# Performance work log

Measured on AMD Instinct MI355X. Metric: run time of the kernel, lower is better.

Reference implementation:

```python
import jax, jax.numpy as jnp
import numpy as np

N_NODES = 10000
N_EDGES = 320000
N_TYPES = 64
EDGE_INV = 8
MULT = 32          # env_embed_multiplicity
LAT = 256          # latent MLP width
SH_DIM = 9         # l = 0,1,2 -> 1+3+5
L_OFF = (0, 1, 4)
L_DIM = (1, 3, 5)
R_MAX = 6.0
POLY_P = 6.0
AVG_NEIGH = 32.0


def _w(key, fan_in, fan_out):
    return jax.random.normal(key, (fan_in, fan_out), jnp.float32) / np.sqrt(fan_in)


def setup_inputs() -> dict:
    key = jax.random.key(0)
    ks = jax.random.split(key, 20)
    return {
        "edge_attr": jax.random.normal(ks[0], (N_EDGES, SH_DIM), jnp.float32),
        "edge_length": jax.random.uniform(ks[1], (N_EDGES,), jnp.float32),
        "edge_invariants": jax.random.normal(ks[2], (N_EDGES, EDGE_INV), jnp.float32),
        "node_invariants": jax.random.uniform(ks[3], (N_NODES, N_TYPES), jnp.float32),
        "W2a": _w(ks[4], 2 * N_TYPES + EDGE_INV, LAT),
        "W2b": _w(ks[5], LAT, LAT),
        "Wl1a": _w(ks[6], LAT + MULT * 3, LAT),
        "Wl1b": _w(ks[7], LAT, LAT),
        "Wenv0": _w(ks[8], LAT, 2 * MULT * 3),
        "Wenv1": _w(ks[9], LAT, MULT * 3),
        "Wenvlin": jax.random.normal(ks[10], (2, 3, MULT, MULT), jnp.float32) / np.sqrt(MULT),
        "Wprod": jax.random.normal(ks[11], (2, 3, N_TYPES, MULT), jnp.float32) / np.sqrt(N_TYPES),
        "Wfeat": jax.random.normal(ks[12], (2, 3, MULT, MULT), jnp.float32) / np.sqrt(MULT),
        "Wfinlat": _w(ks[13], LAT, 3 * MULT * MULT),
        "Wro1": _w(ks[14], LAT + MULT * 3, LAT),
        "Wro2": _w(ks[15], LAT, 1),
        "edge_index": jax.random.randint(ks[16], (2, N_EDGES), 0, N_NODES),
    }


def poly_cutoff(x, p=POLY_P):
    # nequip polynomial cutoff, f(0)=1, f(1)=0 with p continuous derivatives
    f = (1.0 - (p + 1.0) * (p + 2.0) / 2.0 * x ** p
         + p * (p + 2.0) * x ** (p + 1.0)
         - p * (p + 1.0) / 2.0 * x ** (p + 2.0))
    return jnp.where(x < 1.0, f, 0.0)


def weight_channels(sh, w):
    # MakeWeightedChannels: sh [E,9], w [E,K,3 irreps] -> [E,K,9]
    return jnp.concatenate(
        [sh[:, None, o:o + d] * w[:, :, l:l + 1]
         for l, (o, d) in enumerate(zip(L_OFF, L_DIM))], axis=-1)


def mix_channels(x, W):
    # equivariant Linear: per-l channel mixing. x [N,K,9], W [3,K,K]
    return jnp.concatenate(
        [jnp.einsum('nkm,kj->njm', x[:, :, o:o + d], W[l])
         for l, (o, d) in enumerate(zip(L_OFF, L_DIM))], axis=-1)


def l_norms(x):
    # rotation-invariant per-(channel,l) norms: x [E,K,9] -> [E, K*3]
    return jnp.concatenate(
        [jnp.sqrt(jnp.sum(x[:, :, o:o + d] ** 2, axis=-1) + 1e-8)
         for (o, d) in zip(L_OFF, L_DIM)], axis=-1)


def _forward(edge_index, edge_attr, edge_length, edge_invariants, node_invariants,
             W2a, W2b, Wl1a, Wl1b, Wenv0, Wenv1, Wenvlin, Wprod, Wfeat,
             Wfinlat, Wro1, Wro2):
    center, neigh = edge_index[0], edge_index[1]
    n_nodes = node_invariants.shape[0]
    silu = jax.nn.silu
    cutoff = poly_cutoff(edge_length / R_MAX)                  # [E]
    alpha = jax.nn.sigmoid(0.0)                                # resnet update param init 0
    c_old = 1.0 / jnp.sqrt(alpha * alpha + 1.0)
    c_new = alpha * c_old
    norm = 1.0 / AVG_NEIGH                                     # env_sum_normalizations

    def env_and_product(env_w, lidx):
        # weighted SH channels -> scatter-sum env -> env linear -> product basis
        env_e = weight_channels(edge_attr, env_w) * cutoff[:, None, None]   # [E,K,9]
        env = jax.ops.segment_sum(env_e, center, num_segments=n_nodes) * norm
        env = mix_channels(env, Wenvlin[lidx])                  # [N,K,9]
        s = env[:, :, 0:1]                                      # scalar (l=0) channel
        ew = jnp.einsum('nt,ctk->nck', node_invariants, Wprod[lidx])  # element weights [N,3,K]
        prod = env * (ew[:, 0, :, None] + ew[:, 1, :, None] * s + ew[:, 2, :, None] * s * s)
        return mix_channels(prod, Wfeat[lidx])[center]          # gather back to edges [E,K,9]

    # ---- layer 0: two-body latent ----
    lat_in = jnp.concatenate(
        [node_invariants[center], node_invariants[neigh], edge_invariants], axis=-1)
    latents = cutoff[:, None] * silu(silu(lat_in @ W2a) @ W2b)  # [E,LAT]
    w_all = (latents @ Wenv0).reshape(-1, 2, MULT, 3)           # initial + env weights
    features0 = weight_channels(edge_attr, w_all[:, 0])         # initial weighted channels
    features = env_and_product(w_all[:, 1], 0)

    # ---- layer 1: latent resnet update ----
    lat_in = jnp.concatenate([latents, l_norms(features)], axis=-1)
    new_lat = silu(silu(lat_in @ Wl1a) @ Wl1b)
    latents = c_old * latents + c_new * cutoff[:, None] * new_lat
    features = env_and_product((latents @ Wenv1).reshape(-1, MULT, 3), 1)

    # ---- final per-edge linear (weights from latents) + diagonal 'uuu' TP -> invariants ----
    wfin = (latents @ Wfinlat).reshape(-1, 3, MULT, MULT)
    feat_fin = jnp.concatenate(
        [jnp.einsum('ekm,ekj->ejm', features[:, :, o:o + d], wfin[:, l])
         for l, (o, d) in enumerate(zip(L_OFF, L_DIM))], axis=-1)
    scal = jnp.concatenate(
        [jnp.sum(feat_fin[:, :, o:o + d] * features0[:, :, o:o + d], axis=-1)
         for (o, d) in zip(L_OFF, L_DIM)], axis=-1)              # [E, K*3]
    ro_in = jnp.concatenate([latents, scal], axis=-1)
    return silu(ro_in @ Wro1) @ Wro2                             # [E,1] edge energies


def reference(edge_attr, edge_length, edge_invariants, node_invariants,
              W2a, W2b, Wl1a, Wl1b, Wenv0, Wenv1, Wenvlin, Wprod, Wfeat,
              Wfinlat, Wro1, Wro2, edge_index):
    return _forward(edge_index, edge_attr, edge_length, edge_invariants, node_invariants,
                    W2a, W2b, Wl1a, Wl1b, Wenv0, Wenv1, Wenvlin, Wprod, Wfeat,
                    Wfinlat, Wro1, Wro2)
```

## Files before the change

### kernel.cpp

```cpp
#include <hip/hip_runtime.h>
#include <math.h>

#define NE 320000
#define NNODES 10000
#define EB 32
#define NBLK (NE / EB)
#define AST 360
#define BST 264
#define SST 98

typedef _Float16 f16x8 __attribute__((ext_vector_type(8)));
typedef float f32x4 __attribute__((ext_vector_type(4)));
typedef float f32x16 __attribute__((ext_vector_type(16)));

__device__ __forceinline__ float silu(float x) { return x / (1.0f + __expf(-x)); }
__device__ __forceinline__ float cutf(float len) {
    float x = len * (1.0f / 6.0f);
    float x2 = x * x, x6 = x2 * x2 * x2;
    float f = 1.0f - 28.0f * x6 + 48.0f * x6 * x - 21.0f * x6 * x2;
    return (x < 1.0f) ? f : 0.0f;
}

__global__ __launch_bounds__(256) void k_zero(float* __restrict__ p, int n) {
    int i = blockIdx.x * 256 + threadIdx.x;
    if (i < n) p[i] = 0.f;
}

__global__ __launch_bounds__(256) void k_packf(const float* __restrict__ src,
                                               _Float16* __restrict__ dst,
                                               int K, int KS, int NT, int stride,
                                               int colOff) {
    int i = blockIdx.x * 256 + threadIdx.x;
    if (i >= NT * KS * 512) return;
    int j = i & 7, lane = (i >> 3) & 63;
    int blk = i >> 9;
    int ks = blk % KS, nt = blk / KS;
    int k = ks * 32 + (lane >> 4) * 8 + j;
    int n = colOff + nt * 16 + (lane & 15);
    dst[i] = (k < K) ? (_Float16)src[(size_t)k * stride + n] : (_Float16)0.f;
}

__global__ __launch_bounds__(256) void k_packfin3(const float* __restrict__ W,
                                                  _Float16* __restrict__ dst) {
    int i = blockIdx.x * 256 + threadIdx.x;
    int j = i & 7, lane = (i >> 3) & 63, q = (i >> 9) & 15, s = i >> 13;
    int l = s >> 5, ke = s & 31;
    int c = q * 16 + (lane >> 5) * 8 + j;
    int n = l * 1024 + ke * 32 + (lane & 31);
    dst[i] = (_Float16)W[(size_t)c * 3072 + n];
}

__global__ __launch_bounds__(256) void k_packro5(const float* __restrict__ W,
                                                 _Float16* __restrict__ dst) {
    int i = blockIdx.x * 256 + threadIdx.x;
    if (i >= 90112) return;
    int j = i & 7, lane = (i >> 3) & 63, u = i >> 9;
    int cb = u / 22, ks2 = u - cb * 22;
    int k = ks2 * 16 + (lane >> 5) * 8 + j;
    int n = cb * 32 + (lane & 31);
    dst[i] = (_Float16)W[(size_t)k * 256 + n];
}

template <int NT>
__device__ __forceinline__ void mfma_gemm2(int ksteps, const _Float16* Ah, int astride,
                                           const _Float16* __restrict__ Wt, int t,
                                           f32x4* acc0, f32x4* acc1) {
    int wave = t >> 6, lane = t & 63, r = lane & 15, g = lane >> 4;
    const int TPW = (NT + 3) / 4;
#pragma unroll
    for (int i = 0; i < TPW; ++i) {
        acc0[i] = (f32x4){0.f, 0.f, 0.f, 0.f};
        acc1[i] = (f32x4){0.f, 0.f, 0.f, 0.f};
    }
    for (int ks = 0; ks < ksteps; ++ks) {
        f16x8 a0 = *(const f16x8*)(Ah + r * astride + ks * 32 + g * 8);
        f16x8 a1 = *(const f16x8*)(Ah + (16 + r) * astride + ks * 32 + g * 8);
#pragma unroll
        for (int i = 0; i < TPW; ++i) {
            int nt = wave + 4 * i;
            if (nt < NT) {
                f16x8 b = *(const f16x8*)(Wt + ((size_t)(nt * ksteps + ks) * 64 + lane) * 8);
                acc0[i] = __builtin_amdgcn_mfma_f32_16x16x32_f16(a0, b, acc0[i], 0, 0, 0);
                acc1[i] = __builtin_amdgcn_mfma_f32_16x16x32_f16(a1, b, acc1[i], 0, 0, 0);
            }
        }
    }
}

__device__ __forceinline__ void gather_latin(
    const float* __restrict__ nodeinv, const float* __restrict__ edgeinv,
    const float* __restrict__ elen, const int* __restrict__ eidx,
    int e0, int t, _Float16* Ah, float* s_cut) {
    if (t < EB) s_cut[t] = cutf(elen[e0 + t]);
    for (int i = t; i < EB * 160; i += 256) {
        int ee = i / 160, k = i - ee * 160;
        int e = e0 + ee;
        float v;
        if (k < 64)       v = nodeinv[eidx[e] * 64 + k];
        else if (k < 128) v = nodeinv[eidx[NE + e] * 64 + (k - 64)];
        else if (k < 136) v = edgeinv[(size_t)e * 8 + (k - 128)];
        else              v = 0.f;
        Ah[ee * AST + k] = (_Float16)v;
    }
}

__device__ __forceinline__ void lat0_mfma2(const _Float16* __restrict__ W2aT,
                                           const _Float16* __restrict__ W2bT,
                                           int t, _Float16* Ah, _Float16* AhB,
                                           const float* s_cut) {
    int wave = t >> 6, lane = t & 63, r = lane & 15, g = lane >> 4;
    f32x4 acc0[4], acc1[4];
    mfma_gemm2<16>(5, Ah, AST, W2aT, t, acc0, acc1);
#pragma unroll
    for (int i = 0; i < 4; ++i) {
        int nt = wave + 4 * i;
#pragma unroll
        for (int i2 = 0; i2 < 4; ++i2) {
            AhB[(g * 4 + i2) * BST + nt * 16 + r] = (_Float16)silu(acc0[i][i2]);
            AhB[(16 + g * 4 + i2) * BST + nt * 16 + r] = (_Float16)silu(acc1[i][i2]);
        }
    }
    __syncthreads();
    mfma_gemm2<16>(8, AhB, BST, W2bT, t, acc0, acc1);
#pragma unroll
    for (int i = 0; i < 4; ++i) {
        int nt = wave + 4 * i;
#pragma unroll
        for (int i2 = 0; i2 < 4; ++i2) {
            int ro = g * 4 + i2, col = nt * 16 + r;
            Ah[ro * AST + col] = (_Float16)(s_cut[ro] * silu(acc0[i][i2]));
            Ah[(16 + ro) * AST + col] = (_Float16)(s_cut[16 + ro] * silu(acc1[i][i2]));
        }
    }
    __syncthreads();
}

__device__ __forceinline__ void gather_lnorm(const float* __restrict__ featN,
                                             const int* __restrict__ eidx,
                                             int e0, int t, _Float16* Ah) {
    for (int i = t; i < EB * 96; i += 256) {
        int ee = i / 96, rem = i - ee * 96;
        int l = rem >> 5, kk = rem & 31;
        int off = (l == 0) ? 0 : ((l == 1) ? 1 : 4);
        int d = (l == 0) ? 1 : ((l == 1) ? 3 : 5);
        const float* f = featN + (size_t)eidx[e0 + ee] * 288 + kk;
        float s = 1e-8f;
        for (int mm = off; mm < off + d; ++mm) { float x = f[mm * 32]; s = fmaf(x, x, s); }
        Ah[ee * AST + 256 + rem] = (_Float16)sqrtf(s);
    }
}

__device__ __forceinline__ void scatter_env(const float* __restrict__ edge_attr,
                                            const int* __restrict__ eidx,
                                            const float* s_w, const float* s_cut,
                                            int e0, int t, float* __restrict__ env) {
    for (int i = t; i < EB * 32; i += 256) {
        int el = i >> 5, k = i & 31;
        int e = e0 + el;
        float cw = s_cut[el];
        int n = eidx[e];
        float w0 = s_w[el * 96 + k * 3 + 0] * cw;
        float w1 = s_w[el * 96 + k * 3 + 1] * cw;
        float w2 = s_w[el * 96 + k * 3 + 2] * cw;
        float* dst = env + (size_t)n * 288 + k;
#pragma unroll
        for (int m = 0; m < 9; ++m) {
            float w = (m == 0) ? w0 : ((m < 4) ? w1 : w2);
            atomicAdd(dst + m * 32, edge_attr[(size_t)e * 9 + m] * w);
        }
    }
}

__device__ __forceinline__ void epi6_f32(const f32x4* acc0, const f32x4* acc1, int t,
                                         float* s_w) {
    int wave = t >> 6, lane = t & 63, r = lane & 15, g = lane >> 4;
#pragma unroll
    for (int i = 0; i < 2; ++i) {
        int nt = wave + 4 * i;
        if (nt < 6) {
#pragma unroll
            for (int i2 = 0; i2 < 4; ++i2) {
                s_w[(g * 4 + i2) * 96 + nt * 16 + r] = acc0[i][i2];
                s_w[(16 + g * 4 + i2) * 96 + nt * 16 + r] = acc1[i][i2];
            }
        }
    }
}

__global__ __launch_bounds__(256) void k1_lat_scatter0(
    const float* __restrict__ nodeinv, const float* __restrict__ edgeinv,
    const float* __restrict__ elen, const float* __restrict__ edge_attr,
    const int* __restrict__ eidx, const _Float16* __restrict__ W2aT,
    const _Float16* __restrict__ W2bT, const _Float16* __restrict__ Wenv0T,
    float* __restrict__ env, _Float16* __restrict__ lat0h,
    _Float16* __restrict__ w0h) {
    __shared__ alignas(16) _Float16 Ah[EB * AST];
    __shared__ alignas(16) _Float16 AhB[EB * BST];
    __shared__ float s_cut[EB];
    float* s_w = (float*)AhB;
    int t = threadIdx.x;
    int e0 = blockIdx.x * EB;
    int wave = t >> 6, lane = t & 63, r = lane & 15, g = lane >> 4;
    gather_latin(nodeinv, edgeinv, elen, eidx, e0, t, Ah, s_cut);
    __syncthreads();
    lat0_mfma2(W2aT, W2bT, t, Ah, AhB, s_cut);
    for (int i = t; i < EB * 32; i += 256) {
        int ee = i >> 5, c8 = (i & 31) * 8;
        *(f16x8*)(lat0h + (size_t)(e0 + ee) * 256 + c8) =
            *(const f16x8*)(Ah + ee * AST + c8);
    }
    f32x4 acc0[3], acc1[3];
    mfma_gemm2<12>(8, Ah, AST, Wenv0T, t, acc0, acc1);
#pragma unroll
    for (int i = 0; i < 3; ++i) {
        int nt = wave + 4 * i;
        if (nt < 6) {
#pragma unroll
            for (int i2 = 0; i2 < 4; ++i2) {
                w0h[(size_t)(e0 + g * 4 + i2) * 96 + nt * 16 + r] = (_Float16)acc0[i][i2];
                w0h[(size_t)(e0 + 16 + g * 4 + i2) * 96 + nt * 16 + r] = (_Float16)acc1[i][i2];
            }
        } else {
#pragma unroll
            for (int i2 = 0; i2 < 4; ++i2) {
                s_w[(g * 4 + i2) * 96 + (nt - 6) * 16 + r] = acc0[i][i2];
                s_w[(16 + g * 4 + i2) * 96 + (nt - 6) * 16 + r] = acc1[i][i2];
            }
        }
    }
    __syncthreads();
    scatter_env(edge_attr, eidx, s_w, s_cut, e0, t, env);
}

__global__ __launch_bounds__(288) void k_node(
    const float* envin, const float* __restrict__ nodeinv,
    const float* __restrict__ Wenvlin, const float* __restrict__ Wprod,
    const float* __restrict__ Wfeat, float* featOut) {
    __shared__ float s_env[288];
    __shared__ float s_inv[64];
    __shared__ float s_mix[288];
    __shared__ float s_ew[96];
    int n = blockIdx.x;
    int t = threadIdx.x;
    s_env[t] = envin[(size_t)n * 288 + t] * (1.0f / 32.0f);
    if (t < 64) s_inv[t] = nodeinv[n * 64 + t];
    __syncthreads();
    int m = t >> 5, j = t & 31;
    int l = (m == 0) ? 0 : ((m < 4) ? 1 : 2);
    float a = 0.f;
    for (int k = 0; k < 32; ++k) a = fmaf(s_env[m * 32 + k], Wenvlin[l * 1024 + k * 32 + j], a);
    if (t < 96) {
        int c = t >> 5, jj = t & 31;
        float b = 0.f;
        for (int tt = 0; tt < 64; ++tt) b = fmaf(s_inv[tt], Wprod[c * 2048 + tt * 32 + jj], b);
        s_ew[t] = b;
    }
    s_mix[t] = a;
    __syncthreads();
    float s = s_mix[j];
    float p = s_mix[t] * (s_ew[j] + s_ew[32 + j] * s + s_ew[64 + j] * s * s);
    __syncthreads();
    s_env[t] = p;
    __syncthreads();
    float o = 0.f;
    for (int jl = 0; jl < 32; ++jl) o = fmaf(s_env[m * 32 + jl], Wfeat[l * 1024 + jl * 32 + j], o);
    featOut[(size_t)n * 288 + t] = o;
}

__global__ __launch_bounds__(256) void k3_update_scatter1(
    const float* __restrict__ elen, const float* __restrict__ edge_attr,
    const int* __restrict__ eidx, const _Float16* __restrict__ Wl1aT,
    const _Float16* __restrict__ Wl1bT, const _Float16* __restrict__ Wenv1T,
    const float* __restrict__ featN0, float* __restrict__ env,
    _Float16* __restrict__ lat01h) {
    __shared__ alignas(16) _Float16 Ah[EB * AST];
    __shared__ alignas(16) _Float16 AhB[EB * BST];
    __shared__ float s_cut[EB];
    float* s_w = (float*)AhB;
    int t = threadIdx.x;
    int e0 = blockIdx.x * EB;
    int wave = t >> 6, lane = t & 63, r = lane & 15, g = lane >> 4;
    if (t < EB) s_cut[t] = cutf(elen[e0 + t]);
    for (int i = t; i < EB * 32; i += 256) {
        int ee = i >> 5, c8 = (i & 31) * 8;
        *(f16x8*)(Ah + ee * AST + c8) =
            *(const f16x8*)(lat01h + (size_t)(e0 + ee) * 256 + c8);
    }
    gather_lnorm(featN0, eidx, e0, t, Ah);
    __syncthreads();
    f32x4 acc0[4], acc1[4];
    mfma_gemm2<16>(11, Ah, AST, Wl1aT, t, acc0, acc1);
#pragma unroll
    for (int i = 0; i < 4; ++i) {
        int nt = wave + 4 * i;
#pragma unroll
        for (int i2 = 0; i2 < 4; ++i2) {
            AhB[(g * 4 + i2) * BST + nt * 16 + r] = (_Float16)silu(acc0[i][i2]);
            AhB[(16 + g * 4 + i2) * BST + nt * 16 + r] = (_Float16)silu(acc1[i][i2]);
        }
    }
    __syncthreads();
    mfma_gemm2<16>(8, AhB, BST, Wl1bT, t, acc0, acc1);
#pragma unroll
    for (int i = 0; i < 4; ++i) {
        int nt = wave + 4 * i;
#pragma unroll
        for (int i2 = 0; i2 < 4; ++i2) {
            int ro = g * 4 + i2, col = nt * 16 + r;
            float v0 = 0.8944271909999159f * (float)Ah[ro * AST + col] +
                       0.4472135954999579f * s_cut[ro] * silu(acc0[i][i2]);
            _Float16 h0 = (_Float16)v0;
            Ah[ro * AST + col] = h0;
            lat01h[(size_t)(e0 + ro) * 256 + col] = h0;
            float v1 = 0.8944271909999159f * (float)Ah[(16 + ro) * AST + col] +
                       0.4472135954999579f * s_cut[16 + ro] * silu(acc1[i][i2]);
            _Float16 h1 = (_Float16)v1;
            Ah[(16 + ro) * AST + col] = h1;
            lat01h[(size_t)(e0 + 16 + ro) * 256 + col] = h1;
        }
    }
    __syncthreads();
    mfma_gemm2<6>(8, Ah, AST, Wenv1T, t, acc0, acc1);
    epi6_f32(acc0, acc1, t, s_w);
    __syncthreads();
    scatter_env(edge_attr, eidx, s_w, s_cut, e0, t, env);
}

#define FEB 128
__global__ __launch_bounds__(256) void k5_fast(
    const float* __restrict__ edge_attr, const int* __restrict__ eidx,
    const _Float16* __restrict__ lat1h, const _Float16* __restrict__ w0h,
    const _Float16* __restrict__ Bfin3, const _Float16* __restrict__ Wro1T32,
    const float* __restrict__ Wro2, const float* __restrict__ featN1,
    float* __restrict__ out) {
    __shared__ alignas(16) _Float16 Bst[2][8192];
    __shared__ alignas(16) _Float16 s_S[FEB * SST];
    int t = threadIdx.x;
    int e0 = blockIdx.x * FEB;
    int wave = t >> 6, lane = t & 63;
    int r31 = lane & 31, kh5 = lane >> 5;
    for (int i = t; i < FEB * 96; i += 256) {
        int ee = i / 96, rem = i - ee * 96;
        int l = rem >> 5, kk = rem & 31;
        int off = (l == 0) ? 0 : ((l == 1) ? 1 : 4);
        int d = (l == 0) ? 1 : ((l == 1) ? 3 : 5);
        int e = e0 + ee;
        const float* f = featN1 + (size_t)eidx[e] * 288 + kk;
        float s = 0.f;
        for (int mm = off; mm < off + d; ++mm)
            s = fmaf(f[mm * 32], edge_attr[(size_t)e * 9 + mm], s);
        s_S[ee * SST + rem] = (_Float16)s;
    }
    f16x8 a2[16];
#pragma unroll
    for (int q = 0; q < 16; ++q)
        a2[q] = *(const f16x8*)(lat1h + (size_t)(e0 + wave * 32 + r31) * 256 +
                                q * 16 + kh5 * 8);
#pragma unroll
    for (int c = 0; c < 4; ++c) {
        f16x8 gc = *(const f16x8*)(Bfin3 + (size_t)(c * 256 + t) * 8);
        *(f16x8*)&Bst[0][(c * 256 + t) * 8] = gc;
    }
    __syncthreads();
    const f32x16 z16 = {0.f, 0.f, 0.f, 0.f, 0.f, 0.f, 0.f, 0.f,
                        0.f, 0.f, 0.f, 0.f, 0.f, 0.f, 0.f, 0.f};
    f32x16 acc[3];
#pragma unroll
    for (int l = 0; l < 3; ++l) acc[l] = z16;
    int cur = 0;
#pragma unroll
    for (int l = 0; l < 3; ++l) {
#pragma unroll 1
        for (int ke = 0; ke < 32; ++ke) {
            int s = l * 32 + ke;
            f16x8 g0, g1, g2, g3;
            if (s < 95) {
                const _Float16* g = Bfin3 + (size_t)(s + 1) * 8192;
                g0 = *(const f16x8*)(g + (size_t)(0 * 256 + t) * 8);
                g1 = *(const f16x8*)(g + (size_t)(1 * 256 + t) * 8);
                g2 = *(const f16x8*)(g + (size_t)(2 * 256 + t) * 8);
                g3 = *(const f16x8*)(g + (size_t)(3 * 256 + t) * 8);
            }
            _Float16 sh = s_S[(wave * 32 + r31) * SST + l * 32 + ke];
            f16x8 sb = {sh, sh, sh, sh, sh, sh, sh, sh};
#pragma unroll
            for (int q = 0; q < 16; ++q) {
                f16x8 b = *(const f16x8*)&Bst[cur][q * 512 + lane * 8];
                f16x8 ap = a2[q] * sb;
                acc[l] = __builtin_amdgcn_mfma_f32_32x32x16_f16(ap, b, acc[l], 0, 0, 0);
            }
            if (s < 95) {
                *(f16x8*)&Bst[cur ^ 1][(0 * 256 + t) * 8] = g0;
                *(f16x8*)&Bst[cur ^ 1][(1 * 256 + t) * 8] = g1;
                *(f16x8*)&Bst[cur ^ 1][(2 * 256 + t) * 8] = g2;
                *(f16x8*)&Bst[cur ^ 1][(3 * 256 + t) * 8] = g3;
            }
            __syncthreads();
            cur ^= 1;
        }
    }
#pragma unroll
    for (int l = 0; l < 3; ++l) {
#pragma unroll
        for (int reg = 0; reg < 16; ++reg) {
            int row = (reg & 3) + 8 * (reg >> 2) + 4 * kh5;
            int jo = r31;
            float w0 = (float)w0h[(size_t)(e0 + wave * 32 + row) * 96 + jo * 3 + l];
            s_S[(wave * 32 + row) * SST + l * 32 + jo] = (_Float16)(acc[l][reg] * w0);
        }
    }
    __syncthreads();
    float v16[16];
#pragma unroll
    for (int reg = 0; reg < 16; ++reg) v16[reg] = 0.f;
#pragma unroll 1
    for (int cb = 0; cb < 8; ++cb) {
        f32x16 racc = z16;
#pragma unroll
        for (int ks2 = 0; ks2 < 22; ++ks2) {
            f16x8 af = (ks2 < 16)
                ? a2[ks2]
                : *(const f16x8*)&s_S[(wave * 32 + r31) * SST + (ks2 - 16) * 16 + kh5 * 8];
            f16x8 b = *(const f16x8*)(Wro1T32 + ((size_t)(cb * 22 + ks2) * 512 + lane * 8));
            racc = __builtin_amdgcn_mfma_f32_32x32x16_f16(af, b, racc, 0, 0, 0);
        }
        float w2 = Wro2[cb * 32 + r31];
#pragma unroll
        for (int reg = 0; reg < 16; ++reg) v16[reg] += silu(racc[reg]) * w2;
    }
#pragma unroll
    for (int off = 1; off < 32; off <<= 1)
#pragma unroll
        for (int reg = 0; reg < 16; ++reg) v16[reg] += __shfl_xor(v16[reg], off);
    if (r31 == 0) {
#pragma unroll
        for (int reg = 0; reg < 16; ++reg) {
            int row = (reg & 3) + 8 * (reg >> 2) + 4 * kh5;
            out[e0 + wave * 32 + row] = v16[reg];
        }
    }
}

extern "C" void kernel_launch(void* const* d_in, const int* in_sizes, int n_in,
                              void* d_out, int out_size, void* d_ws, size_t ws_size,
                              hipStream_t stream) {
    (void)in_sizes; (void)n_in; (void)out_size;
    const float* edge_attr = (const float*)d_in[0];
    const float* edge_len  = (const float*)d_in[1];
    const float* edge_inv  = (const float*)d_in[2];
    const float* node_inv  = (const float*)d_in[3];
    const float* W2a     = (const float*)d_in[4];
    const float* W2b     = (const float*)d_in[5];
    const float* Wl1a    = (const float*)d_in[6];
    const float* Wl1b    = (const float*)d_in[7];
    const float* Wenv0   = (const float*)d_in[8];
    const float* Wenv1   = (const float*)d_in[9];
    const float* Wenvlin = (const float*)d_in[10];
    const float* Wprod   = (const float*)d_in[11];
    const float* Wfeat   = (const float*)d_in[12];
    const float* Wfinlat = (const float*)d_in[13];
    const float* Wro1    = (const float*)d_in[14];
    const float* Wro2    = (const float*)d_in[15];
    const int* eidx      = (const int*)d_in[16];
    float* out = (float*)d_out;

    _Float16* p = (_Float16*)d_ws;
    _Float16* Bfin3   = p; p += 786432;
    _Float16* W2aT    = p; p += 40960;
    _Float16* W2bT    = p; p += 65536;
    _Float16* Wenv0T  = p; p += 49152;
    _Float16* Wenv1T  = p; p += 24576;
    _Float16* Wl1aT   = p; p += 90112;
    _Float16* Wl1bT   = p; p += 65536;
    _Float16* Wro1T32 = p; p += 90112;
    float* env    = (float*)p;
    float* featN0 = env + (size_t)NNODES * 288;
    char* after = (char*)(featN0 + (size_t)NNODES * 288);
    size_t need_base = (size_t)(after - (char*)d_ws);
    if (ws_size < need_base) return;
    _Float16* lat01h = (_Float16*)after;
    _Float16* w0h    = lat01h + (size_t)NE * 256;
    size_t need = need_base + (size_t)NE * (256 + 96) * sizeof(_Float16);
    if (ws_size < need) return;

    const int ENV_N = NNODES * 288;
    k_packfin3<<<3072, 256, 0, stream>>>(Wfinlat, Bfin3);
    k_packf<<<160, 256, 0, stream>>>(W2a, W2aT, 136, 5, 16, 256, 0);
    k_packf<<<256, 256, 0, stream>>>(W2b, W2bT, 256, 8, 16, 256, 0);
    k_packf<<<192, 256, 0, stream>>>(Wenv0, Wenv0T, 256, 8, 12, 192, 0);
    k_packf<<<96, 256, 0, stream>>>(Wenv1, Wenv1T, 256, 8, 6, 96, 0);
    k_packf<<<352, 256, 0, stream>>>(Wl1a, Wl1aT, 352, 11, 16, 256, 0);
    k_packf<<<256, 256, 0, stream>>>(Wl1b, Wl1bT, 256, 8, 16, 256, 0);
    k_packro5<<<352, 256, 0, stream>>>(Wro1, Wro1T32);

    k_zero<<<(ENV_N + 255) / 256, 256, 0, stream>>>(env, ENV_N);
    k1_lat_scatter0<<<NBLK, 256, 0, stream>>>(node_inv, edge_inv, edge_len, edge_attr,
                                              eidx, W2aT, W2bT, Wenv0T, env, lat01h, w0h);
    k_node<<<NNODES, 288, 0, stream>>>(env, node_inv, Wenvlin, Wprod, Wfeat, featN0);
    k_zero<<<(ENV_N + 255) / 256, 256, 0, stream>>>(env, ENV_N);
    k3_update_scatter1<<<NBLK, 256, 0, stream>>>(edge_len, edge_attr, eidx,
                                                 Wl1aT, Wl1bT, Wenv1T, featN0, env, lat01h);
    k_node<<<NNODES, 288, 0, stream>>>(env, node_inv, Wenvlin + 3072, Wprod + 6144,
                                       Wfeat + 3072, env);
    k5_fast<<<NE / FEB, 256, 0, stream>>>(edge_attr, eidx, lat01h, w0h, Bfin3, Wro1T32,
                                          Wro2, env, out);
}
```

Measured before the change: 2.684 ms.

## Sort edges by source node to cut scatter atomics via segmented reduction

Adds a counting sort of edges by source node (histogram, scan, place), so every edge kernel works in sorted order. The env scatter in k1 and k3 then does a run-length segmented reduction in shared memory and issues one atomic per node run instead of one per edge. The goal is fewer global atomics and more locality in the gathers. The k5 inner loop is also changed to apply the per-channel scalar in fp32 after the MFMA, not by scaling the fp16 operand. The cost is extra sort kernels, indirect index loads, and a serial single-block scan.

New measurement: 2.685 ms, median of 2. About the same (+0.0%).

```diff
diff --git a/kernel.cpp b/kernel.cpp
--- a/kernel.cpp
+++ b/kernel.cpp
@@ -24,6 +24,54 @@
 __global__ __launch_bounds__(256) void k_zero(float* __restrict__ p, int n) {
     int i = blockIdx.x * 256 + threadIdx.x;
     if (i < n) p[i] = 0.f;
+}
+
+__global__ __launch_bounds__(256) void k_hist(const int* __restrict__ eidx,
+                                              int* __restrict__ cnt) {
+    int e = blockIdx.x * 256 + threadIdx.x;
+    if (e < NE) atomicAdd(&cnt[eidx[e]], 1);
+}
+
+__global__ __launch_bounds__(256) void k_scan(const int* __restrict__ cnt,
+                                              int* __restrict__ seg,
+                                              int* __restrict__ cursor) {
+    __shared__ int part[256];
+    __shared__ int base[256];
+    int t = threadIdx.x;
+    int start = t * 40;
+    int s = 0;
+    for (int i = 0; i < 40; ++i) {
+        int idx = start + i;
+        if (idx < NNODES) s += cnt[idx];
+    }
+    part[t] = s;
+    __syncthreads();
+    if (t == 0) {
+        int run = 0;
+        for (int i = 0; i < 256; ++i) { base[i] = run; run += part[i]; }
+    }
+    __syncthreads();
+    int run = base[t];
+    for (int i = 0; i < 40; ++i) {
+        int idx = start + i;
+        if (idx < NNODES) {
+            int c = cnt[idx];
+            seg[idx] = run;
+            cursor[idx] = run;
+            run += c;
+        }
+    }
+    if (t == 0) seg[NNODES] = NE;
+}
+
+__global__ __launch_bounds__(256) void k_place(const int* __restrict__ eidx,
+                                               int* __restrict__ cursor,
+                                               int* __restrict__ eord) {
+    int e = blockIdx.x * 256 + threadIdx.x;
+    if (e < NE) {
+        int p = atomicAdd(&cursor[eidx[e]], 1);
+        eord[p] = e;
+    }
 }
 
 __global__ __launch_bounds__(256) void k_packf(const float* __restrict__ src,
@@ -90,11 +138,14 @@
 __device__ __forceinline__ void gather_latin(
     const float* __restrict__ nodeinv, const float* __restrict__ edgeinv,
     const float* __restrict__ elen, const int* __restrict__ eidx,
-    int e0, int t, _Float16* Ah, float* s_cut) {
-    if (t < EB) s_cut[t] = cutf(elen[e0 + t]);
+    const int* __restrict__ eord, int e0, int t, _Float16* Ah, float* s_cut) {
+    if (t < EB) {
+        int e = eord ? eord[e0 + t] : (e0 + t);
+        s_cut[t] = cutf(elen[e]);
+    }
     for (int i = t; i < EB * 160; i += 256) {
         int ee = i / 160, k = i - ee * 160;
-        int e = e0 + ee;
+        int e = eord ? eord[e0 + ee] : (e0 + ee);
         float v;
         if (k < 64)       v = nodeinv[eidx[e] * 64 + k];
         else if (k < 128) v = nodeinv[eidx[NE + e] * 64 + (k - 64)];
@@ -137,13 +188,15 @@
 
 __device__ __forceinline__ void gather_lnorm(const float* __restrict__ featN,
                                              const int* __restrict__ eidx,
+                                             const int* __restrict__ eord,
                                              int e0, int t, _Float16* Ah) {
     for (int i = t; i < EB * 96; i += 256) {
         int ee = i / 96, rem = i - ee * 96;
         int l = rem >> 5, kk = rem & 31;
         int off = (l == 0) ? 0 : ((l == 1) ? 1 : 4);
         int d = (l == 0) ? 1 : ((l == 1) ? 3 : 5);
-        const float* f = featN + (size_t)eidx[e0 + ee] * 288 + kk;
+        int e = eord ? eord[e0 + ee] : (e0 + ee);
+        const float* f = featN + (size_t)eidx[e] * 288 + kk;
         float s = 1e-8f;
         for (int mm = off; mm < off + d; ++mm) { float x = f[mm * 32]; s = fmaf(x, x, s); }
         Ah[ee * AST + 256 + rem] = (_Float16)sqrtf(s);
@@ -171,6 +224,27 @@
     }
 }
 
+__device__ __forceinline__ void scatter_sorted(const float* s_sh, const int* s_nid,
+                                               const float* s_w, int t,
+                                               float* __restrict__ env) {
+    for (int pp = t; pp < 288; pp += 256) {
+        int m = pp >> 5, k = pp & 31;
+        int l = (m == 0) ? 0 : ((m < 4) ? 1 : 2);
+        float run = 0.f;
+        int nprev = s_nid[0];
+        for (int el = 0; el < EB; ++el) {
+            int nid = s_nid[el];
+            if (nid != nprev) {
+                atomicAdd(&env[(size_t)nprev * 288 + m * 32 + k], run);
+                run = 0.f;
+                nprev = nid;
+            }
+            run = fmaf(s_sh[el * 9 + m], s_w[el * 96 + k * 3 + l], run);
+        }
+        atomicAdd(&env[(size_t)nprev * 288 + m * 32 + k], run);
+    }
+}
+
 __device__ __forceinline__ void epi6_f32(const f32x4* acc0, const f32x4* acc1, int t,
                                          float* s_w) {
     int wave = t >> 6, lane = t & 63, r = lane & 15, g = lane >> 4;
@@ -193,15 +267,17 @@
     const int* __restrict__ eidx, const _Float16* __restrict__ W2aT,
     const _Float16* __restrict__ W2bT, const _Float16* __restrict__ Wenv0T,
     float* __restrict__ env, _Float16* __restrict__ lat0h,
-    _Float16* __restrict__ w0h) {
+    _Float16* __restrict__ w0h, const int* __restrict__ eord) {
     __shared__ alignas(16) _Float16 Ah[EB * AST];
     __shared__ alignas(16) _Float16 AhB[EB * BST];
     __shared__ float s_cut[EB];
+    __shared__ float s_sh[EB * 9];
+    __shared__ int s_nid[EB];
     float* s_w = (float*)AhB;
     int t = threadIdx.x;
     int e0 = blockIdx.x * EB;
     int wave = t >> 6, lane = t & 63, r = lane & 15, g = lane >> 4;
-    gather_latin(nodeinv, edgeinv, elen, eidx, e0, t, Ah, s_cut);
+    gather_latin(nodeinv, edgeinv, elen, eidx, eord, e0, t, Ah, s_cut);
     __syncthreads();
     lat0_mfma2(W2aT, W2bT, t, Ah, AhB, s_cut);
     for (int i = t; i < EB * 32; i += 256) {
@@ -228,8 +304,16 @@
             }
         }
     }
-    __syncthreads();
-    scatter_env(edge_attr, eidx, s_w, s_cut, e0, t, env);
+    if (eord) {
+        if (t < EB) s_nid[t] = eidx[eord[e0 + t]];
+        for (int i = t; i < EB * 9; i += 256) {
+            int el = i / 9, m = i - el * 9;
+            s_sh[i] = edge_attr[(size_t)eord[e0 + el] * 9 + m] * s_cut[el];
+        }
+    }
+    __syncthreads();
+    if (eord) scatter_sorted(s_sh, s_nid, s_w, t, env);
+    else      scatter_env(edge_attr, eidx, s_w, s_cut, e0, t, env);
 }
 
 __global__ __launch_bounds__(288) void k_node(
@@ -272,21 +356,26 @@
     const int* __restrict__ eidx, const _Float16* __restrict__ Wl1aT,
     const _Float16* __restrict__ Wl1bT, const _Float16* __restrict__ Wenv1T,
     const float* __restrict__ featN0, float* __restrict__ env,
-    _Float16* __restrict__ lat01h) {
+    _Float16* __restrict__ lat01h, const int* __restrict__ eord) {
     __shared__ alignas(16) _Float16 Ah[EB * AST];
     __shared__ alignas(16) _Float16 AhB[EB * BST];
     __shared__ float s_cut[EB];
+    __shared__ float s_sh[EB * 9];
+    __shared__ int s_nid[EB];
     float* s_w = (float*)AhB;
     int t = threadIdx.x;
     int e0 = blockIdx.x * EB;
     int wave = t >> 6, lane = t & 63, r = lane & 15, g = lane >> 4;
-    if (t < EB) s_cut[t] = cutf(elen[e0 + t]);
+    if (t < EB) {
+        int e = eord ? eord[e0 + t] : (e0 + t);
+        s_cut[t] = cutf(elen[e]);
+    }
     for (int i = t; i < EB * 32; i += 256) {
         int ee = i >> 5, c8 = (i & 31) * 8;
         *(f16x8*)(Ah + ee * AST + c8) =
             *(const f16x8*)(lat01h + (size_t)(e0 + ee) * 256 + c8);
     }
-    gather_lnorm(featN0, eidx, e0, t, Ah);
+    gather_lnorm(featN0, eidx, eord, e0, t, Ah);
     __syncthreads();
     f32x4 acc0[4], acc1[4];
     mfma_gemm2<16>(11, Ah, AST, Wl1aT, t, acc0, acc1);
@@ -322,8 +411,16 @@
     __syncthreads();
     mfma_gemm2<6>(8, Ah, AST, Wenv1T, t, acc0, acc1);
     epi6_f32(acc0, acc1, t, s_w);
-    __syncthreads();
-    scatter_env(edge_attr, eidx, s_w, s_cut, e0, t, env);
+    if (eord) {
+        if (t < EB) s_nid[t] = eidx[eord[e0 + t]];
+        for (int i = t; i < EB * 9; i += 256) {
+            int el = i / 9, m = i - el * 9;
+            s_sh[i] = edge_attr[(size_t)eord[e0 + el] * 9 + m] * s_cut[el];
+        }
+    }
+    __syncthreads();
+    if (eord) scatter_sorted(s_sh, s_nid, s_w, t, env);
+    else      scatter_env(edge_attr, eidx, s_w, s_cut, e0, t, env);
 }
 
 #define FEB 128
@@ -332,7 +429,7 @@
     const _Float16* __restrict__ lat1h, const _Float16* __restrict__ w0h,
     const _Float16* __restrict__ Bfin3, const _Float16* __restrict__ Wro1T32,
     const float* __restrict__ Wro2, const float* __restrict__ featN1,
-    float* __restrict__ out) {
+    const int* __restrict__ eord, float* __restrict__ out) {
     __shared__ alignas(16) _Float16 Bst[2][8192];
     __shared__ alignas(16) _Float16 s_S[FEB * SST];
     int t = threadIdx.x;
@@ -344,7 +441,7 @@
         int l = rem >> 5, kk = rem & 31;
         int off = (l == 0) ? 0 : ((l == 1) ? 1 : 4);
         int d = (l == 0) ? 1 : ((l == 1) ? 3 : 5);
-        int e = e0 + ee;
+        int e = eord ? eord[e0 + ee] : (e0 + ee);
         const float* f = featN1 + (size_t)eidx[e] * 288 + kk;
         float s = 0.f;
         for (int mm = off; mm < off + d; ++mm)
@@ -381,14 +478,16 @@
                 g2 = *(const f16x8*)(g + (size_t)(2 * 256 + t) * 8);
                 g3 = *(const f16x8*)(g + (size_t)(3 * 256 + t) * 8);
             }
-            _Float16 sh = s_S[(wave * 32 + r31) * SST + l * 32 + ke];
-            f16x8 sb = {sh, sh, sh, sh, sh, sh, sh, sh};
+            float sf = (float)s_S[(wave * 32 + r31) * SST + l * 32 + ke];
+            f32x16 ac = z16;
 #pragma unroll
             for (int q = 0; q < 16; ++q) {
-                f16x8 b = *(const f16x8*)&Bst[cur][q * 512 + lane * 8];
-                f16x8 ap = a2[q] * sb;
-                acc[l] = __builtin_amdgcn_mfma_f32_32x32x16_f16(ap, b, acc[l], 0, 0, 0);
-            }
+                f16x8 bf = *(const f16x8*)&Bst[cur][q * 512 + lane * 8];
+                ac = __builtin_amdgcn_mfma_f32_32x32x16_f16(bf, a2[q], ac, 0, 0, 0);
+            }
+#pragma unroll
+            for (int reg = 0; reg < 16; ++reg)
+                acc[l][reg] = fmaf(sf, ac[reg], acc[l][reg]);
             if (s < 95) {
                 *(f16x8*)&Bst[cur ^ 1][(0 * 256 + t) * 8] = g0;
                 *(f16x8*)&Bst[cur ^ 1][(1 * 256 + t) * 8] = g1;
@@ -399,14 +498,14 @@
             cur ^= 1;
         }
     }
+    int pe = e0 + wave * 32 + r31;
 #pragma unroll
     for (int l = 0; l < 3; ++l) {
 #pragma unroll
         for (int reg = 0; reg < 16; ++reg) {
-            int row = (reg & 3) + 8 * (reg >> 2) + 4 * kh5;
-            int jo = r31;
-            float w0 = (float)w0h[(size_t)(e0 + wave * 32 + row) * 96 + jo * 3 + l];
-            s_S[(wave * 32 + row) * SST + l * 32 + jo] = (_Float16)(acc[l][reg] * w0);
+            int jrow = (reg & 3) + 8 * (reg >> 2) + 4 * kh5;
+            float w0 = (float)w0h[(size_t)pe * 96 + jrow * 3 + l];
+            s_S[(wave * 32 + r31) * SST + l * 32 + jrow] = (_Float16)(acc[l][reg] * w0);
         }
     }
     __syncthreads();
@@ -436,7 +535,9 @@
 #pragma unroll
         for (int reg = 0; reg < 16; ++reg) {
             int row = (reg & 3) + 8 * (reg >> 2) + 4 * kh5;
-            out[e0 + wave * 32 + row] = v16[reg];
+            int pidx = e0 + wave * 32 + row;
+            int e = eord ? eord[pidx] : pidx;
+            out[e] = v16[reg];
         }
     }
 }
@@ -482,6 +583,12 @@
     _Float16* w0h    = lat01h + (size_t)NE * 256;
     size_t need = need_base + (size_t)NE * (256 + 96) * sizeof(_Float16);
     if (ws_size < need) return;
+    int* eord   = (int*)((char*)d_ws + need);
+    int* seg    = eord + NE;
+    int* cursor = seg + NNODES + 1;
+    size_t need_sorted = need + (size_t)(NE + 2 * NNODES + 1) * sizeof(int);
+    bool sorted = (ws_size >= need_sorted);
+    const int* eordk = sorted ? eord : nullptr;
 
     const int ENV_N = NNODES * 288;
     k_packfin3<<<3072, 256, 0, stream>>>(Wfinlat, Bfin3);
@@ -493,15 +600,24 @@
     k_packf<<<256, 256, 0, stream>>>(Wl1b, Wl1bT, 256, 8, 16, 256, 0);
     k_packro5<<<352, 256, 0, stream>>>(Wro1, Wro1T32);
 
+    if (sorted) {
+        k_zero<<<(NNODES + 255) / 256, 256, 0, stream>>>((float*)cursor, NNODES);
+        k_hist<<<NE / 256, 256, 0, stream>>>(eidx, cursor);
+        k_scan<<<1, 256, 0, stream>>>(cursor, seg, cursor);
+        k_place<<<NE / 256, 256, 0, stream>>>(eidx, cursor, eord);
+    }
+
     k_zero<<<(ENV_N + 255) / 256, 256, 0, stream>>>(env, ENV_N);
     k1_lat_scatter0<<<NBLK, 256, 0, stream>>>(node_inv, edge_inv, edge_len, edge_attr,
-                                              eidx, W2aT, W2bT, Wenv0T, env, lat01h, w0h);
+                                              eidx, W2aT, W2bT, Wenv0T, env, lat01h, w0h,
+                                              eordk);
     k_node<<<NNODES, 288, 0, stream>>>(env, node_inv, Wenvlin, Wprod, Wfeat, featN0);
     k_zero<<<(ENV_N + 255) / 256, 256, 0, stream>>>(env, ENV_N);
     k3_update_scatter1<<<NBLK, 256, 0, stream>>>(edge_len, edge_attr, eidx,
-                                                 Wl1aT, Wl1bT, Wenv1T, featN0, env, lat01h);
+                                                 Wl1aT, Wl1bT, Wenv1T, featN0, env, lat01h,
+                                                 eordk);
     k_node<<<NNODES, 288, 0, stream>>>(env, node_inv, Wenvlin + 3072, Wprod + 6144,
                                        Wfeat + 3072, env);
     k5_fast<<<NE / FEB, 256, 0, stream>>>(edge_attr, eidx, lat01h, w0h, Bfin3, Wro1T32,
-                                          Wro2, env, out);
-}
+                                          Wro2, env, eordk, out);
+}
```
